# Kernel optimization log

Measured on AMD Instinct MI355X. Metric: run time of the kernel, lower is better.

Reference implementation:

```python
import jax, jax.numpy as jnp
import numpy as np

MARGIN = 1.0


def setup_inputs() -> dict:
    key = jax.random.key(0)
    k1, k2 = jax.random.split(key)
    B, D = 512, 128
    embeddings = jax.random.normal(k1, (B, D), dtype=jnp.float32)
    labels = jax.random.randint(k2, (B,), 0, 8, dtype=jnp.int64)
    return {"embeddings": embeddings, "labels": labels}


def _triplet_loss(embeddings, labels, margin=MARGIN):
    B = embeddings.shape[0]
    # pairwise euclidean distances (cdist p=2)
    sq = jnp.sum(embeddings * embeddings, axis=1)
    d2 = sq[:, None] + sq[None, :] - 2.0 * (embeddings @ embeddings.T)
    dist = jnp.sqrt(jnp.maximum(d2, 0.0))  # [B, B]

    same = labels[:, None] == labels[None, :]
    eye = jnp.eye(B, dtype=bool)
    pos_mask = same & ~eye          # [B, B] valid positives per anchor
    neg_mask = ~same                # [B, B] valid negatives per anchor
    has_neg = jnp.any(neg_mask, axis=1)  # [B]

    rows = jnp.arange(B)
    # hardest negative per anchor (fallback when no semi-hard negative exists)
    hard_idx = jnp.argmin(jnp.where(neg_mask, dist, jnp.inf), axis=1)  # [B]

    keys = jax.random.split(jax.random.key(42), B)  # one key per positive index p

    def step(carry, xs):
        p, k = xs
        loss_sum, cnt = carry
        pos_d = dist[:, p]                               # [B] anchor->positive dist
        valid = pos_mask[:, p] & has_neg                 # anchor i uses p as positive
        # semi-hard: negative strictly between pos_d and pos_d + margin
        sh = neg_mask & (dist > pos_d[:, None]) & (dist < pos_d[:, None] + margin)
        has_sh = jnp.any(sh, axis=1)
        # uniform random choice among semi-hard negatives via gumbel-argmax
        g = jax.random.gumbel(k, (B, B), dtype=jnp.float32)
        sel = jnp.argmax(jnp.where(sh, g, -jnp.inf), axis=1)
        idx = jnp.where(has_sh, sel, hard_idx)           # [B] chosen negative
        neg_d = dist[rows, idx]
        tl = jax.nn.relu(pos_d - neg_d + margin)
        m = valid & (tl > 0)
        loss_sum = loss_sum + jnp.sum(jnp.where(m, tl, 0.0))
        cnt = cnt + jnp.sum(m.astype(jnp.int32))
        return (loss_sum, cnt), None

    init = (jnp.float32(0.0), jnp.int32(0))
    (loss_sum, cnt), _ = jax.lax.scan(step, init, (rows, keys))
    return jnp.where(cnt == 0, jnp.float32(0.0), loss_sum / cnt.astype(jnp.float32))


def reference(embeddings, labels):
    return _triplet_loss(embeddings, labels)
```

## Files before the change

kernel.cpp:

```cpp
#include <hip/hip_runtime.h>
#include <stdint.h>

#define B 512
#define D 128
#define HALFC 131072u
#define SUB 2
#define NSLOT (SUB * 8)
#define NPART (B * SUB)

__device__ __forceinline__ uint32_t rotl32(uint32_t x, uint32_t r) {
  return (x << r) | (x >> (32u - r));
}

__device__ __forceinline__ void threefry2x32(uint32_t k0, uint32_t k1,
                                             uint32_t x0, uint32_t x1,
                                             uint32_t& y0, uint32_t& y1) {
  uint32_t k2 = k0 ^ k1 ^ 0x1BD11BDAu;
  x0 += k0; x1 += k1;
#define TF_R(r) { x0 += x1; x1 = rotl32(x1, r); x1 ^= x0; }
  TF_R(13) TF_R(15) TF_R(26) TF_R(6)
  x0 += k1; x1 += k2 + 1u;
  TF_R(17) TF_R(29) TF_R(16) TF_R(24)
  x0 += k2; x1 += k0 + 2u;
  TF_R(13) TF_R(15) TF_R(26) TF_R(6)
  x0 += k0; x1 += k1 + 3u;
  TF_R(17) TF_R(29) TF_R(16) TF_R(24)
  x0 += k1; x1 += k2 + 4u;
  TF_R(13) TF_R(15) TF_R(26) TF_R(6)
  x0 += k2; x1 += k0 + 5u;
#undef TF_R
  y0 = x0; y1 = x1;
}

template <int N>
__device__ __forceinline__ void tf_multi(uint32_t k0, uint32_t k1,
                                         uint32_t (&x0)[N], uint32_t (&x1)[N]) {
  uint32_t k2 = k0 ^ k1 ^ 0x1BD11BDAu;
#pragma unroll
  for (int q = 0; q < N; ++q) { x0[q] += k0; x1[q] += k1; }
#define TFM_R(r) \
  _Pragma("unroll") for (int q = 0; q < N; ++q) { \
    x0[q] += x1[q]; x1[q] = rotl32(x1[q], r); x1[q] ^= x0[q]; }
#define TFM_INJ(a, b, c) \
  _Pragma("unroll") for (int q = 0; q < N; ++q) { x0[q] += a; x1[q] += b + c; }
  TFM_R(13) TFM_R(15) TFM_R(26) TFM_R(6)
  TFM_INJ(k1, k2, 1u)
  TFM_R(17) TFM_R(29) TFM_R(16) TFM_R(24)
  TFM_INJ(k2, k0, 2u)
  TFM_R(13) TFM_R(15) TFM_R(26) TFM_R(6)
  TFM_INJ(k0, k1, 3u)
  TFM_R(17) TFM_R(29) TFM_R(16) TFM_R(24)
  TFM_INJ(k1, k2, 4u)
  TFM_R(13) TFM_R(15) TFM_R(26) TFM_R(6)
  TFM_INJ(k2, k0, 5u)
#undef TFM_R
#undef TFM_INJ
}

__device__ __forceinline__ uint32_t dpp_max_all(uint32_t x) {
  uint32_t t;
#define DPP_STEP(ctrl) \
  t = (uint32_t)__builtin_amdgcn_update_dpp(0, (int)x, ctrl, 0xf, 0xf, true); \
  x = (t > x) ? t : x;
  DPP_STEP(0x111)
  DPP_STEP(0x112)
  DPP_STEP(0x114)
  DPP_STEP(0x118)
  DPP_STEP(0x142)
  DPP_STEP(0x143)
#undef DPP_STEP
  return (uint32_t)__builtin_amdgcn_readlane((int)x, 63);
}

__global__ __launch_bounds__(256) void dist_kernel(
    const float* __restrict__ emb, float* __restrict__ dist,
    uint32_t* __restrict__ keys0, uint32_t* __restrict__ keys1) {
  __shared__ float As[32][132];
  __shared__ float Bs[32][132];
  __shared__ float sqa[32], sqb[32];
  int bid = blockIdx.x;
  int ti = bid >> 4, tj = bid & 15;
  int t = threadIdx.x;

  const float4* ga = reinterpret_cast<const float4*>(emb + (size_t)ti * 32 * D);
  const float4* gb = reinterpret_cast<const float4*>(emb + (size_t)tj * 32 * D);
  #pragma unroll
  for (int k = 0; k < 4; ++k) {
    int idx = t + k * 256;
    int r = idx >> 5;
    int c4 = idx & 31;
    *reinterpret_cast<float4*>(&As[r][c4 * 4]) = ga[idx];
    *reinterpret_cast<float4*>(&Bs[r][c4 * 4]) = gb[idx];
  }
  __syncthreads();

  {
    int row = t >> 2, seg = t & 3;
    const float* src = (row < 32) ? &As[row][seg * 32] : &Bs[row - 32][seg * 32];
    float s = 0.f;
    #pragma unroll
    for (int m = 0; m < 32; ++m) { float v = src[m]; s += v * v; }
    s += __shfl_xor(s, 1);
    s += __shfl_xor(s, 2);
    if (seg == 0) { if (row < 32) sqa[row] = s; else sqb[row - 32] = s; }
  }

  int r = t >> 3, g = t & 7;
  const float4* A4 = reinterpret_cast<const float4*>(&As[r][0]);
  const float4* B0 = reinterpret_cast<const float4*>(&Bs[g][0]);
  const float4* B1 = reinterpret_cast<const float4*>(&Bs[g + 8][0]);
  const float4* B2 = reinterpret_cast<const float4*>(&Bs[g + 16][0]);
  const float4* B3 = reinterpret_cast<const float4*>(&Bs[g + 24][0]);
  float acc0 = 0.f, acc1 = 0.f, acc2 = 0.f, acc3 = 0.f;
  #pragma unroll 8
  for (int k4 = 0; k4 < 32; ++k4) {
    float4 a = A4[k4];
    float4 b0 = B0[k4], b1 = B1[k4], b2 = B2[k4], b3 = B3[k4];
    acc0 += a.x * b0.x + a.y * b0.y + a.z * b0.z + a.w * b0.w;
    acc1 += a.x * b1.x + a.y * b1.y + a.z * b1.z + a.w * b1.w;
    acc2 += a.x * b2.x + a.y * b2.y + a.z * b2.z + a.w * b2.w;
    acc3 += a.x * b3.x + a.y * b3.y + a.z * b3.z + a.w * b3.w;
  }
  __syncthreads();
  float sa = sqa[r];
  float* drow = dist + (size_t)(ti * 32 + r) * B + tj * 32;
  drow[g]      = sqrtf(fmaxf(sa + sqb[g]      - 2.f * acc0, 0.f));
  drow[g + 8]  = sqrtf(fmaxf(sa + sqb[g + 8]  - 2.f * acc1, 0.f));
  drow[g + 16] = sqrtf(fmaxf(sa + sqb[g + 16] - 2.f * acc2, 0.f));
  drow[g + 24] = sqrtf(fmaxf(sa + sqb[g + 24] - 2.f * acc3, 0.f));

  if (bid == 0) {
    #pragma unroll
    for (int pp = 0; pp < 2; ++pp) {
      int p = t + pp * 256;
      uint32_t i0 = 2u * (uint32_t)p, i1 = i0 + 1u;
      uint32_t a0, a1, b0, b1;
      if (p < 256) {
        threefry2x32(0u, 42u, i0, i0 + 512u, a0, a1);
        threefry2x32(0u, 42u, i1, i1 + 512u, b0, b1);
        keys0[p] = a0; keys1[p] = b0;
      } else {
        threefry2x32(0u, 42u, i0 - 512u, i0, a0, a1);
        threefry2x32(0u, 42u, i1 - 512u, i1, b0, b1);
        keys0[p] = a1; keys1[p] = b1;
      }
    }
  }
}

__global__ __launch_bounds__(512) void triplet_kernel(
    const float* __restrict__ dist, const int* __restrict__ labels,
    const uint32_t* __restrict__ keys0, const uint32_t* __restrict__ keys1,
    double* __restrict__ partials, int* __restrict__ pcnt) {
  __shared__ float drow[B];
  __shared__ unsigned short slab[B];
  __shared__ uint2 skeys[B];
  __shared__ unsigned short list_sh[B];
  __shared__ unsigned short cand[8][B];
  __shared__ int nlist_sh;
  __shared__ double lsum[8];
  __shared__ unsigned int lcnt[8];

  int bid = blockIdx.x;
  int i = bid >> 1;
  int sub = bid & 1;
  int t = threadIdx.x;
  slab[t] = (unsigned short)labels[t];
  drow[t] = dist[(size_t)i * B + t];
  skeys[t] = make_uint2(keys0[t], keys1[t]);
  __syncthreads();

  int wave = t >> 6, lane = t & 63;
  unsigned long long lmask_lt = (1ull << lane) - 1ull;
  unsigned short lab_i = slab[i];

  if (wave == 0) {
    int n = 0;
    #pragma unroll
    for (int c = 0; c < 8; ++c) {
      int r = c * 64 + lane;
      bool v = (slab[r] == lab_i);
      unsigned long long mk = __ballot(v);
      if (v) list_sh[n + __popcll(mk & lmask_lt)] = (unsigned short)r;
      n += __popcll(mk);
    }
    if (lane == 0) nlist_sh = (n == B) ? 0 : n;
  }

  float dd8m[8];
  unsigned long long hkey = ~0ull;
  #pragma unroll
  for (int jc = 0; jc < 8; ++jc) {
    int j = jc * 64 + lane;
    float dv = drow[j];
    bool neg = (slab[j] != lab_i);
    dd8m[jc] = neg ? dv : -3.0e38f;
    if (neg) {
      unsigned long long k =
          (((unsigned long long)__float_as_uint(dv)) << 9) | (unsigned)j;
      if (k < hkey) hkey = k;
    }
  }
  #pragma unroll
  for (int off = 32; off; off >>= 1) {
    unsigned long long o = __shfl_xor(hkey, off);
    if (o < hkey) hkey = o;
  }
  int hard = (int)(hkey & 0x1FFu);
  uint32_t rowbase = (uint32_t)((i & 255) * B);
  bool take_hi = (i >= 256);
  __syncthreads();

  int nlist = nlist_sh;
  unsigned short* wcand = cand[wave];
  double wsum = 0.0;
  unsigned int wcnt = 0;

#define LOAD_ANCHOR(KK, KP, PD) { \
    int p_ = list_sh[KK]; \
    p_ = __builtin_amdgcn_readfirstlane(p_); \
    KP = skeys[p_]; \
    PD = (p_ == i) ? -2.0f : drow[p_];  }

#define DRAIN(NCH) { \
    uint32_t xs0[NCH], xs1[NCH], js[NCH]; \
    _Pragma("unroll") for (int q = 0; q < NCH; ++q) { \
      int c_ = c0 + q * 64; \
      uint32_t j_ = wcand[(c_ < nc) ? c_ : 0]; \
      js[q] = j_; \
      xs0[q] = rowbase + j_; \
      xs1[q] = rowbase + j_ + HALFC; \
    } \
    tf_multi<NCH>(kp.x, kp.y, xs0, xs1); \
    _Pragma("unroll") for (int q = 0; q < NCH; ++q) { \
      int c_ = c0 + q * 64; \
      uint32_t kk = ((take_hi ? xs1[q] : xs0[q]) & 0xFFFFFE00u) | \
                    (511u - js[q]); \
      if (c_ < nc && kk > best) best = kk; \
    } }

  int k = sub * 8 + wave;
  uint2 kpN; float pdN;
  if (k < nlist) LOAD_ANCHOR(k, kpN, pdN);

  while (k < nlist) {
    uint2 kp = kpN;
    float pos_d = pdN;
    int kn = k + NSLOT;
    if (kn < nlist) LOAD_ANCHOR(kn, kpN, pdN);
    float hiv = pos_d + 1.0f;

    int nc = 0;
    #pragma unroll
    for (int jc = 0; jc < 8; ++jc) {
      float dd = dd8m[jc];
      bool m = (dd > pos_d) && (dd < hiv);
      unsigned long long mk = __ballot(m);
      if (m) wcand[nc + __popcll(mk & lmask_lt)] =
          (unsigned short)(jc * 64 + lane);
      nc += __popcll(mk);
    }

    float tl;
    if (nc > 0) {
      uint32_t best = 0u;
      int nch = (nc + 63) >> 6;
      int c0 = lane;
      while (nch > 4) { DRAIN(4); c0 += 256; nch -= 4; }
      switch (nch) {
        case 4: DRAIN(4); break;
        case 3: DRAIN(3); break;
        case 2: DRAIN(2); break;
        default: DRAIN(1); break;
      }
      best = dpp_max_all(best);
      int idx = 511 - (int)(best & 0x1FFu);
      tl = pos_d - drow[idx] + 1.0f;
    } else {
      tl = pos_d - drow[hard] + 1.0f;
    }
    if (tl > 0.f) { wsum += (double)tl; wcnt++; }
    k = kn;
  }
#undef LOAD_ANCHOR
#undef DRAIN

  if (lane == 0) { lsum[wave] = wsum; lcnt[wave] = wcnt; }
  __syncthreads();
  if (t == 0) {
    double s = 0.0;
    unsigned int c = 0;
    #pragma unroll
    for (int w = 0; w < 8; ++w) { s += lsum[w]; c += lcnt[w]; }
    partials[bid] = s;
    pcnt[bid] = (int)c;
  }
}

__global__ __launch_bounds__(256) void finalize_kernel(
    const double* __restrict__ partials, const int* __restrict__ pcnt,
    float* __restrict__ out) {
  __shared__ double ss[256];
  __shared__ int sc[256];
  int t = threadIdx.x;
  double s = 0.0;
  int c = 0;
  for (int k = t; k < NPART; k += 256) { s += partials[k]; c += pcnt[k]; }
  ss[t] = s; sc[t] = c;
  __syncthreads();
  for (int st = 128; st; st >>= 1) {
    if (t < st) { ss[t] += ss[t + st]; sc[t] += sc[t + st]; }
    __syncthreads();
  }
  if (t == 0) out[0] = sc[0] ? (float)(ss[0] / (double)sc[0]) : 0.0f;
}

extern "C" void kernel_launch(void* const* d_in, const int* in_sizes, int n_in,
                              void* d_out, int out_size, void* d_ws, size_t ws_size,
                              hipStream_t stream) {
  const float* emb = (const float*)d_in[0];
  const int* labels = (const int*)d_in[1];
  float* out = (float*)d_out;
  char* ws = (char*)d_ws;

  float* dist = (float*)ws;
  uint32_t* keys0 = (uint32_t*)(ws + 1048576);
  uint32_t* keys1 = (uint32_t*)(ws + 1048576 + 2048);
  double* partials = (double*)(ws + 1048576 + 4096);
  int* pcnt = (int*)(ws + 1048576 + 4096 + 8192);

  dist_kernel<<<256, 256, 0, stream>>>(emb, dist, keys0, keys1);
  triplet_kernel<<<B * SUB, 512, 0, stream>>>(dist, labels, keys0, keys1,
                                              partials, pcnt);
  finalize_kernel<<<1, 256, 0, stream>>>(partials, pcnt, out);
}
```

Baseline: 36.89 us.

## Bucket-sort negatives by distance to scan only the semi-hard range

```diff
diff --git a/kernel.cpp b/kernel.cpp
--- a/kernel.cpp
+++ b/kernel.cpp
@@ -156,7 +156,12 @@
   __shared__ unsigned short slab[B];
   __shared__ uint2 skeys[B];
   __shared__ unsigned short list_sh[B];
-  __shared__ unsigned short cand[8][B];
+  __shared__ uint32_t hist[B];
+  __shared__ uint32_t offs[B];
+  __shared__ uint32_t cur[B];
+  __shared__ unsigned long long skey_arr[B];
+  __shared__ uint32_t wsum32[8];
+  __shared__ uint32_t wprefix[8];
   __shared__ int nlist_sh;
   __shared__ double lsum[8];
   __shared__ unsigned int lcnt[8];
@@ -168,6 +173,7 @@
   slab[t] = (unsigned short)labels[t];
   drow[t] = dist[(size_t)i * B + t];
   skeys[t] = make_uint2(keys0[t], keys1[t]);
+  hist[t] = 0u;
   __syncthreads();
 
   int wave = t >> 6, lane = t & 63;
@@ -187,18 +193,20 @@
     if (lane == 0) nlist_sh = (n == B) ? 0 : n;
   }
 
-  float dd8m[8];
+  float dv_t = drow[t];
+  bool neg_t = (slab[t] != lab_i);
+  int b_t = (int)fminf(fmaxf(dv_t * 16.0f, 0.0f), 511.0f);
+  if (neg_t) atomicAdd(&hist[b_t], 1u);
+
   unsigned long long hkey = ~0ull;
   #pragma unroll
   for (int jc = 0; jc < 8; ++jc) {
     int j = jc * 64 + lane;
     float dv = drow[j];
-    bool neg = (slab[j] != lab_i);
-    dd8m[jc] = neg ? dv : -3.0e38f;
-    if (neg) {
-      unsigned long long k =
+    if (slab[j] != lab_i) {
+      unsigned long long kk =
           (((unsigned long long)__float_as_uint(dv)) << 9) | (unsigned)j;
-      if (k < hkey) hkey = k;
+      if (kk < hkey) hkey = kk;
     }
   }
   #pragma unroll
@@ -207,12 +215,36 @@
     if (o < hkey) hkey = o;
   }
   int hard = (int)(hkey & 0x1FFu);
+  __syncthreads();
+
+  uint32_t v = hist[t];
+  #pragma unroll
+  for (int d = 1; d < 64; d <<= 1) {
+    uint32_t u = __shfl_up(v, d);
+    if (lane >= (unsigned)d) v += u;
+  }
+  if (lane == 63) wsum32[wave] = v;
+  __syncthreads();
+  if (t == 0) {
+    uint32_t acc = 0;
+    #pragma unroll
+    for (int w = 0; w < 8; ++w) { wprefix[w] = acc; acc += wsum32[w]; }
+  }
+  __syncthreads();
+  uint32_t inc = v + wprefix[wave];
+  offs[t] = inc;
+  cur[t] = inc - hist[t];
+  __syncthreads();
+  if (neg_t) {
+    uint32_t pos = atomicAdd(&cur[b_t], 1u);
+    skey_arr[pos] =
+        (((unsigned long long)__float_as_uint(dv_t)) << 9) | (unsigned)t;
+  }
   uint32_t rowbase = (uint32_t)((i & 255) * B);
   bool take_hi = (i >= 256);
   __syncthreads();
 
   int nlist = nlist_sh;
-  unsigned short* wcand = cand[wave];
   double wsum = 0.0;
   unsigned int wcnt = 0;
 
@@ -223,20 +255,20 @@
     PD = (p_ == i) ? -2.0f : drow[p_];  }
 
 #define DRAIN(NCH) { \
-    uint32_t xs0[NCH], xs1[NCH], js[NCH]; \
+    uint32_t xs0[NCH], xs1[NCH], js[NCH]; bool vd[NCH]; \
     _Pragma("unroll") for (int q = 0; q < NCH; ++q) { \
       int c_ = c0 + q * 64; \
-      uint32_t j_ = wcand[(c_ < nc) ? c_ : 0]; \
-      js[q] = j_; \
-      xs0[q] = rowbase + j_; \
-      xs1[q] = rowbase + j_ + HALFC; \
+      unsigned long long kv = skey_arr[(c_ < end) ? c_ : start]; \
+      vd[q] = (c_ < end) && (kv > lokey) && (kv < hikey); \
+      js[q] = (uint32_t)(kv & 0x1FFu); \
+      xs0[q] = rowbase + js[q]; \
+      xs1[q] = rowbase + js[q] + HALFC; \
     } \
     tf_multi<NCH>(kp.x, kp.y, xs0, xs1); \
     _Pragma("unroll") for (int q = 0; q < NCH; ++q) { \
-      int c_ = c0 + q * 64; \
       uint32_t kk = ((take_hi ? xs1[q] : xs0[q]) & 0xFFFFFE00u) | \
                     (511u - js[q]); \
-      if (c_ < nc && kk > best) best = kk; \
+      if (vd[q] && kk > best) best = kk; \
     } }
 
   int k = sub * 8 + wave;
@@ -248,24 +280,22 @@
     float pos_d = pdN;
     int kn = k + NSLOT;
     if (kn < nlist) LOAD_ANCHOR(kn, kpN, pdN);
-    float hiv = pos_d + 1.0f;
-
-    int nc = 0;
-    #pragma unroll
-    for (int jc = 0; jc < 8; ++jc) {
-      float dd = dd8m[jc];
-      bool m = (dd > pos_d) && (dd < hiv);
-      unsigned long long mk = __ballot(m);
-      if (m) wcand[nc + __popcll(mk & lmask_lt)] =
-          (unsigned short)(jc * 64 + lane);
-      nc += __popcll(mk);
-    }
+    float hi_f = pos_d + 1.0f;
+
+    int lo_b = (int)fminf(fmaxf(pos_d * 16.0f, 0.0f), 511.0f);
+    int hi_b = (int)fminf(fmaxf(hi_f * 16.0f, 0.0f), 511.0f);
+    int start = (int)(offs[lo_b] - hist[lo_b]);
+    int end = (int)offs[hi_b];
+    unsigned long long lokey =
+        (((unsigned long long)__float_as_uint(pos_d)) << 9) | 511u;
+    unsigned long long hikey =
+        ((unsigned long long)__float_as_uint(hi_f)) << 9;
 
     float tl;
-    if (nc > 0) {
+    if (end > start) {
       uint32_t best = 0u;
-      int nch = (nc + 63) >> 6;
-      int c0 = lane;
+      int nch = (end - start + 63) >> 6;
+      int c0 = start + lane;
       while (nch > 4) { DRAIN(4); c0 += 256; nch -= 4; }
       switch (nch) {
         case 4: DRAIN(4); break;
@@ -274,7 +304,7 @@
         default: DRAIN(1); break;
       }
       best = dpp_max_all(best);
-      int idx = 511 - (int)(best & 0x1FFu);
+      int idx = best ? (511 - (int)(best & 0x1FFu)) : hard;
       tl = pos_d - drow[idx] + 1.0f;
     } else {
       tl = pos_d - drow[hard] + 1.0f;
```

Result: no change. 36.41 us (-1.3%).
